# Optimization experiments

Hardware: AMD Instinct MI355X
Metric: run time of the kernel (lower is better)

Reference implementation:

```python
import jax, jax.numpy as jnp
import numpy as np

WS = 7  # window_size
NH = 8  # num_heads

def _rel_pos_index(ws):
    coords = np.stack(np.meshgrid(np.arange(ws), np.arange(ws), indexing='ij'))  # [2,ws,ws]
    flat = coords.reshape(2, -1)                      # [2, ws*ws]
    rel = (flat[:, :, None] - flat[:, None, :]).transpose(1, 2, 0)  # [ws*ws, ws*ws, 2]
    rel = rel + (ws - 1)
    rel[:, :, 0] *= 2 * ws - 1
    return rel.sum(-1)  # [ws*ws, ws*ws]

REL_IDX = jnp.asarray(_rel_pos_index(WS))


def setup_inputs() -> dict:
    key = jax.random.key(0)
    k1, k2, k3 = jax.random.split(key, 3)
    B, H, W, C = 4, 224, 224, 256
    x = jax.random.normal(k1, (B, H * W, C), dtype=jnp.float32)
    nW = (H // WS) * (W // WS)
    mask = jnp.zeros((nW, WS * WS, WS * WS), dtype=jnp.float32)
    qkv_w = jax.random.normal(k2, (3 * C, C), dtype=jnp.float32) * 0.02
    qkv_b = jnp.zeros((3 * C,), dtype=jnp.float32)
    rel_bias_table = jax.random.normal(k3, ((2 * WS - 1) ** 2, NH), dtype=jnp.float32) * 0.02
    return {"x": x, "mask": mask, "qkv_w": qkv_w, "qkv_b": qkv_b,
            "rel_bias_table": rel_bias_table, "H": H, "W": W}


def reference(x, mask, qkv_w, qkv_b, rel_bias_table, H, W):
    B, N, C = x.shape
    nh = rel_bias_table.shape[1]
    hd = C // nh
    scale = hd ** (-0.5)
    shift = WS // 2

    qkv = x @ qkv_w.T + qkv_b                       # [B, N, 3C]
    q = qkv.reshape(B, H, W, 3 * C)
    pad_h = (WS - H % WS) % WS
    pad_w = (WS - W % WS) % WS
    if pad_h or pad_w:
        q = jnp.pad(q, ((0, 0), (0, pad_h), (0, pad_w), (0, 0)))
    Hp, Wp = H + pad_h, W + pad_w

    # mask is provided -> shifted-window path (cyclic shift)
    q = jnp.roll(q, (-shift, -shift), axis=(1, 2))

    nWh, nWw = Hp // WS, Wp // WS
    win = q.reshape(B, nWh, WS, nWw, WS, 3 * C).transpose(0, 1, 3, 2, 4, 5)
    win = win.reshape(B * nWh * nWw, WS * WS, 3, nh, hd).transpose(2, 0, 3, 1, 4)
    qh, kh, vh = win[0], win[1], win[2]             # each [B_, nh, 49, hd]

    attn = jnp.einsum('bhqd,bhkd->bhqk', qh, kh) * scale
    bias = rel_bias_table[REL_IDX.reshape(-1)].reshape(WS * WS, WS * WS, nh)
    attn = attn + bias.transpose(2, 0, 1)[None]     # [B_, nh, 49, 49]

    nW = mask.shape[0]
    attn = attn.reshape(B, nW, nh, WS * WS, WS * WS) + mask[None, :, None]
    attn = jax.nn.softmax(attn.reshape(-1, nh, WS * WS, WS * WS), axis=-1)

    out = jnp.einsum('bhqk,bhkd->bhqd', attn, vh)   # [B_, nh, 49, hd]
    out = out.transpose(0, 2, 1, 3).reshape(-1, WS * WS, C)

    # window reverse
    out = out.reshape(B, nWh, nWw, WS, WS, C).transpose(0, 1, 3, 2, 4, 5)
    out = out.reshape(B, Hp, Wp, C)
    out = jnp.roll(out, (shift, shift), axis=(1, 2))
    return out.reshape(B, Hp * Wp, C)[:, :N, :]
```

## Files before the change

kernel.cpp:

```cpp
#include <hip/hip_runtime.h>
#include <hip/hip_bf16.h>

#define NTOK  49
#define CDIM  256
#define NHD   8
#define HDIM  32
#define HP    224
#define WPW   224
#define SHIFT 3

typedef __attribute__((ext_vector_type(8))) short short8;
typedef __attribute__((ext_vector_type(4))) short short4v;
typedef __attribute__((ext_vector_type(4))) float float4v;

static __device__ __forceinline__ short f2bf(float f) {
    unsigned u = __float_as_uint(f);
    u += 0x7FFF + ((u >> 16) & 1);
    return (short)(u >> 16);
}

__global__ void cvt_w_kernel(const float* __restrict__ w, short* __restrict__ wb) {
    int t = blockIdx.x * 256 + threadIdx.x;
    float4v f = *(const float4v*)(w + (size_t)t * 4);
    short4v o;
    o.x = f2bf(f.x); o.y = f2bf(f.y); o.z = f2bf(f.z); o.w = f2bf(f.w);
    *(short4v*)(wb + (size_t)t * 4) = o;
}

struct __align__(16) SMem {
    int   nsrc[64];
    short xs[8 * 49 * 40];
    float btabt[8 * 169];
    float pad_[8];
    struct {
        union {
            struct { short q[49 * 40]; short k[49 * 40]; } qk;
            short p[64 * 40];
            float o[49 * 36];
        } r1;
        short vT[32 * 72];
    } wv[2];
};

__global__ __launch_bounds__(128, 1)
void swin_attn_kernel(const float* __restrict__ x,
                      const float* __restrict__ mask,
                      const float* __restrict__ qkv_b,
                      const float* __restrict__ btab,
                      const short* __restrict__ wb,
                      float* __restrict__ out)
{
    __shared__ SMem S;

    const int tid = threadIdx.x;
    const int blk = blockIdx.x;
    const int b   = blk >> 10;
    const int wi  = blk & 1023;
    const int wh  = wi >> 5, ww = wi & 31;

    if (tid < NTOK) {
        int i = tid / 7, j = tid - i * 7;
        int hs = wh * 7 + i + SHIFT;  if (hs >= HP)  hs -= HP;
        int wsx = ww * 7 + j + SHIFT; if (wsx >= WPW) wsx -= WPW;
        S.nsrc[tid] = hs * WPW + wsx;
    }
    for (int idx = tid; idx < 1152; idx += 128) {
        ((int*)S.wv[0].vT)[idx] = 0;
        ((int*)S.wv[1].vT)[idx] = 0;
    }
    __syncthreads();

    const size_t xbase = (size_t)b * (HP * WPW) * CDIM;
    for (int idx = tid; idx < NTOK * 64; idx += 128) {
        int r = idx >> 6, k4 = idx & 63;
        float4v f = *(const float4v*)(x + xbase + (size_t)S.nsrc[r] * CDIM + k4 * 4);
        short4v o4;
        o4.x = f2bf(f.x); o4.y = f2bf(f.y); o4.z = f2bf(f.z); o4.w = f2bf(f.w);
        int kt = k4 >> 3, kk = (k4 & 7) * 4;
        *(short4v*)&S.xs[(kt * 49 + r) * 40 + kk] = o4;
    }
    for (int idx = tid; idx < 1352; idx += 128) {
        int h2 = idx & 7, bi = idx >> 3;
        S.btabt[h2 * 169 + bi] = btab[idx];
    }
    __syncthreads();

    const int lane = tid & 63;
    const int w    = tid >> 6;
    const int n16  = lane & 15;
    const int quad = lane >> 4;
    const float scale = 0.17677669529663687f;

    auto& W = S.wv[w];

    int rt[4][4], ct[4];
#pragma unroll
    for (int mt = 0; mt < 4; ++mt)
#pragma unroll
        for (int reg = 0; reg < 4; ++reg) {
            int r = mt * 16 + quad * 4 + reg;
            int i1 = r / 7;
            rt[mt][reg] = i1 * 13 + (r - i1 * 7);
        }
#pragma unroll
    for (int nt = 0; nt < 4; ++nt) {
        int c = nt * 16 + n16;
        int i2 = c / 7;
        ct[nt] = i2 * 13 + (c - i2 * 7) - 84;
    }

    float mreg[4][4][4];
    {
        const float* maskp = mask + (size_t)wi * 2401;
#pragma unroll
        for (int mt = 0; mt < 4; ++mt)
#pragma unroll
            for (int reg = 0; reg < 4; ++reg) {
                int r  = mt * 16 + quad * 4 + reg;
                int rm = (r < NTOK) ? r : (NTOK - 1);
#pragma unroll
                for (int nt = 0; nt < 4; ++nt) {
                    int c  = nt * 16 + n16;
                    int cm = (c < NTOK) ? c : (NTOK - 1);
                    mreg[mt][nt][reg] = maskp[rm * 49 + cm];
                }
            }
    }

#pragma unroll 1
    for (int h = w * 4; h < w * 4 + 4; ++h) {
        const short* bp[6];
        float bias[6];
#pragma unroll
        for (int i = 0; i < 6; ++i) {
            int chan = (i >> 1) * 256 + h * 32 + (i & 1) * 16 + n16;
            bp[i]   = wb + (size_t)chan * 256 + quad * 8;
            bias[i] = qkv_b[chan];
        }
        float4v acc[4][6];
#pragma unroll
        for (int mt = 0; mt < 4; ++mt)
#pragma unroll
            for (int i = 0; i < 6; ++i)
                acc[mt][i] = (float4v)0.0f;

#pragma unroll
        for (int kt = 0; kt < 8; ++kt) {
            short8 a[4];
#pragma unroll
            for (int mt = 0; mt < 4; ++mt)
                a[mt] = *(const short8*)&S.xs[(kt * 49 + mt * 16 + n16) * 40 + quad * 8];
#pragma unroll
            for (int i = 0; i < 6; ++i) {
                short8 bb = *(const short8*)(bp[i] + kt * 32);
#pragma unroll
                for (int mt = 0; mt < 4; ++mt)
                    acc[mt][i] = __builtin_amdgcn_mfma_f32_16x16x32_bf16(a[mt], bb, acc[mt][i], 0, 0, 0);
            }
        }

#pragma unroll
        for (int mt = 0; mt < 4; ++mt)
#pragma unroll
            for (int reg = 0; reg < 4; ++reg) {
                int r = mt * 16 + quad * 4 + reg;
                if (r < NTOK) {
#pragma unroll
                    for (int i = 0; i < 6; ++i) {
                        float v = acc[mt][i][reg] + bias[i];
                        int c = (i & 1) * 16 + n16;
                        if ((i >> 1) == 0)      W.r1.qk.q[r * 40 + c] = f2bf(v * scale);
                        else if ((i >> 1) == 1) W.r1.qk.k[r * 40 + c] = f2bf(v);
                        else                    W.vT[c * 72 + r]      = f2bf(v);
                    }
                }
            }
        __syncthreads();

        short8 aq[4], bk[4];
#pragma unroll
        for (int t = 0; t < 4; ++t) {
            aq[t] = *(const short8*)&W.r1.qk.q[(t * 16 + n16) * 40 + quad * 8];
            bk[t] = *(const short8*)&W.r1.qk.k[(t * 16 + n16) * 40 + quad * 8];
        }
        float4v sa[4][4];
#pragma unroll
        for (int mt = 0; mt < 4; ++mt)
#pragma unroll
            for (int nt = 0; nt < 4; ++nt)
                sa[mt][nt] = __builtin_amdgcn_mfma_f32_16x16x32_bf16(aq[mt], bk[nt], (float4v)0.0f, 0, 0, 0);

        const float* bt = &S.btabt[h * 169];
#pragma unroll
        for (int mt = 0; mt < 4; ++mt)
#pragma unroll
            for (int nt = 0; nt < 4; ++nt)
#pragma unroll
                for (int reg = 0; reg < 4; ++reg) {
                    float sv;
                    if (nt == 3 && n16 >= 1) sv = -1e30f;
                    else {
                        int bidx = rt[mt][reg] - ct[nt];
                        bidx = (bidx > 168) ? 168 : bidx;
                        sv = sa[mt][nt][reg] + bt[bidx] + mreg[mt][nt][reg];
                    }
                    sa[mt][nt][reg] = sv;
                }

#pragma unroll
        for (int mt = 0; mt < 4; ++mt)
#pragma unroll
            for (int reg = 0; reg < 4; ++reg) {
                float m0 = fmaxf(fmaxf(sa[mt][0][reg], sa[mt][1][reg]),
                                 fmaxf(sa[mt][2][reg], sa[mt][3][reg]));
#pragma unroll
                for (int d = 1; d < 16; d <<= 1) m0 = fmaxf(m0, __shfl_xor(m0, d));
                float s0 = 0.f;
#pragma unroll
                for (int nt = 0; nt < 4; ++nt) {
                    float e = __expf(sa[mt][nt][reg] - m0);
                    sa[mt][nt][reg] = e;
                    s0 += e;
                }
#pragma unroll
                for (int d = 1; d < 16; d <<= 1) s0 += __shfl_xor(s0, d);
                float inv = 1.0f / s0;
#pragma unroll
                for (int nt = 0; nt < 4; ++nt) sa[mt][nt][reg] *= inv;
            }

#pragma unroll
        for (int mt = 0; mt < 4; ++mt)
#pragma unroll
            for (int reg = 0; reg < 4; ++reg) {
                int q = mt * 16 + quad * 4 + reg;
                W.r1.p[q * 40 + n16]      = f2bf(sa[mt][0][reg]);
                W.r1.p[q * 40 + 16 + n16] = f2bf(sa[mt][1][reg]);
            }
        __syncthreads();

        float4v oa[2][4];
#pragma unroll
        for (int mtv = 0; mtv < 2; ++mtv)
#pragma unroll
            for (int nt = 0; nt < 4; ++nt)
                oa[mtv][nt] = (float4v)0.0f;

        {
            short8 av[2], bpv[4];
#pragma unroll
            for (int mtv = 0; mtv < 2; ++mtv)
                av[mtv] = *(const short8*)&W.vT[(mtv * 16 + n16) * 72 + quad * 8];
#pragma unroll
            for (int nt = 0; nt < 4; ++nt)
                bpv[nt] = *(const short8*)&W.r1.p[(nt * 16 + n16) * 40 + quad * 8];
#pragma unroll
            for (int mtv = 0; mtv < 2; ++mtv)
#pragma unroll
                for (int nt = 0; nt < 4; ++nt)
                    oa[mtv][nt] = __builtin_amdgcn_mfma_f32_16x16x32_bf16(av[mtv], bpv[nt], oa[mtv][nt], 0, 0, 0);
        }
        __syncthreads();

#pragma unroll
        for (int mt = 0; mt < 4; ++mt)
#pragma unroll
            for (int reg = 0; reg < 4; ++reg) {
                int q = mt * 16 + quad * 4 + reg;
                W.r1.p[q * 40 + n16]      = f2bf(sa[mt][2][reg]);
                W.r1.p[q * 40 + 16 + n16] = f2bf(sa[mt][3][reg]);
            }
        __syncthreads();

        {
            short8 av[2], bpv[4];
#pragma unroll
            for (int mtv = 0; mtv < 2; ++mtv)
                av[mtv] = *(const short8*)&W.vT[(mtv * 16 + n16) * 72 + 32 + quad * 8];
#pragma unroll
            for (int nt = 0; nt < 4; ++nt)
                bpv[nt] = *(const short8*)&W.r1.p[(nt * 16 + n16) * 40 + quad * 8];
#pragma unroll
            for (int mtv = 0; mtv < 2; ++mtv)
#pragma unroll
                for (int nt = 0; nt < 4; ++nt)
                    oa[mtv][nt] = __builtin_amdgcn_mfma_f32_16x16x32_bf16(av[mtv], bpv[nt], oa[mtv][nt], 0, 0, 0);
        }
        __syncthreads();

#pragma unroll
        for (int mtv = 0; mtv < 2; ++mtv)
#pragma unroll
            for (int nt = 0; nt < 4; ++nt)
#pragma unroll
                for (int reg = 0; reg < 4; ++reg) {
                    int qv = nt * 16 + n16;
                    if (qv < NTOK)
                        W.r1.o[qv * 36 + mtv * 16 + quad * 4 + reg] = oa[mtv][nt][reg];
                }
        __syncthreads();
#pragma unroll
        for (int it = 0; it < 7; ++it) {
            int idx = it * 64 + lane;
            if (idx < NTOK * 8) {
                int tok = idx >> 3, c8 = idx & 7;
                float4v ov = *(const float4v*)&W.r1.o[tok * 36 + c8 * 4];
                *(float4v*)(out + xbase + (size_t)S.nsrc[tok] * CDIM + h * HDIM + c8 * 4) = ov;
            }
        }
        __syncthreads();
    }
}

extern "C" void kernel_launch(void* const* d_in, const int* in_sizes, int n_in,
                              void* d_out, int out_size, void* d_ws, size_t ws_size,
                              hipStream_t stream) {
    const float* x      = (const float*)d_in[0];
    const float* mask   = (const float*)d_in[1];
    const float* qkv_w  = (const float*)d_in[2];
    const float* qkv_b  = (const float*)d_in[3];
    const float* btab   = (const float*)d_in[4];
    float* out = (float*)d_out;
    short* wb  = (short*)d_ws;

    cvt_w_kernel<<<dim3(192), dim3(256), 0, stream>>>(qkv_w, wb);
    swin_attn_kernel<<<dim3(4096), dim3(128), 0, stream>>>(
        x, mask, qkv_b, btab, wb, out);
}
```

Before: 950.1 us.

## Make waves independent, swizzle LDS tiles, transpose score layout for in-thread softmax

Each wave now works only on its own LDS region, so block-wide __syncthreads calls between per-head stages become compiler-only memory fences. The attention scores are computed as K·Qᵀ so that most of each softmax reduction happens inside a thread, with only two cross-lane shuffles. The full 64-wide P tile is written once instead of in two halves. The x tile and the P tile use XOR swizzling to cut LDS bank conflicts, and the bias table is stored in LDS as bf16. The risks are correctness that now depends on in-order LDS access within a wave, and small precision loss in the relative position bias.

```diff
diff --git a/kernel.cpp b/kernel.cpp
--- a/kernel.cpp
+++ b/kernel.cpp
@@ -13,10 +13,15 @@
 typedef __attribute__((ext_vector_type(4))) short short4v;
 typedef __attribute__((ext_vector_type(4))) float float4v;
 
+#define MEMFENCE asm volatile("" ::: "memory")
+
 static __device__ __forceinline__ short f2bf(float f) {
     unsigned u = __float_as_uint(f);
     u += 0x7FFF + ((u >> 16) & 1);
     return (short)(u >> 16);
+}
+static __device__ __forceinline__ float bf2f(unsigned short s) {
+    return __uint_as_float((unsigned)s << 16);
 }
 
 __global__ void cvt_w_kernel(const float* __restrict__ w, short* __restrict__ wb) {
@@ -29,13 +34,12 @@
 
 struct __align__(16) SMem {
     int   nsrc[64];
-    short xs[8 * 49 * 40];
-    float btabt[8 * 169];
-    float pad_[8];
-    struct {
+    short xs[8 * 49 * 32];
+    unsigned short btabt[8 * 169];
+    struct WV {
         union {
             struct { short q[49 * 40]; short k[49 * 40]; } qk;
-            short p[64 * 40];
+            short p[64 * 64];
             float o[49 * 36];
         } r1;
         short vT[32 * 72];
@@ -58,16 +62,17 @@
     const int wi  = blk & 1023;
     const int wh  = wi >> 5, ww = wi & 31;
 
+    const int lane = tid & 63;
+    const int w    = tid >> 6;
+    SMem::WV& W = S.wv[w];
+
     if (tid < NTOK) {
         int i = tid / 7, j = tid - i * 7;
         int hs = wh * 7 + i + SHIFT;  if (hs >= HP)  hs -= HP;
         int wsx = ww * 7 + j + SHIFT; if (wsx >= WPW) wsx -= WPW;
         S.nsrc[tid] = hs * WPW + wsx;
     }
-    for (int idx = tid; idx < 1152; idx += 128) {
-        ((int*)S.wv[0].vT)[idx] = 0;
-        ((int*)S.wv[1].vT)[idx] = 0;
-    }
+    for (int i2 = lane; i2 < 1152; i2 += 64) ((int*)W.vT)[i2] = 0;
     __syncthreads();
 
     const size_t xbase = (size_t)b * (HP * WPW) * CDIM;
@@ -76,53 +81,51 @@
         float4v f = *(const float4v*)(x + xbase + (size_t)S.nsrc[r] * CDIM + k4 * 4);
         short4v o4;
         o4.x = f2bf(f.x); o4.y = f2bf(f.y); o4.z = f2bf(f.z); o4.w = f2bf(f.w);
-        int kt = k4 >> 3, kk = (k4 & 7) * 4;
-        *(short4v*)&S.xs[(kt * 49 + r) * 40 + kk] = o4;
+        int kt = k4 >> 3;
+        int iu = ((k4 >> 1) & 3) ^ ((r >> 1) & 3) ^ ((kt >> 1) & 3);
+        *(short4v*)&S.xs[((kt * 49 + r) << 5) + (iu << 3) + ((k4 & 1) << 2)] = o4;
     }
     for (int idx = tid; idx < 1352; idx += 128) {
         int h2 = idx & 7, bi = idx >> 3;
-        S.btabt[h2 * 169 + bi] = btab[idx];
+        S.btabt[h2 * 169 + bi] = (unsigned short)f2bf(btab[idx]);
     }
     __syncthreads();
 
-    const int lane = tid & 63;
-    const int w    = tid >> 6;
     const int n16  = lane & 15;
     const int quad = lane >> 4;
+    const int rs   = (n16 >> 1) & 3;
     const float scale = 0.17677669529663687f;
 
-    auto& W = S.wv[w];
-
-    int rt[4][4], ct[4];
-#pragma unroll
-    for (int mt = 0; mt < 4; ++mt)
+    int qv[4], kv[4][4];
+#pragma unroll
+    for (int ct = 0; ct < 4; ++ct) {
+        int qq = ct * 16 + n16;
+        int qi = qq / 7;
+        qv[ct] = qi * 13 + (qq - qi * 7);
+    }
+#pragma unroll
+    for (int rt = 0; rt < 4; ++rt)
 #pragma unroll
         for (int reg = 0; reg < 4; ++reg) {
-            int r = mt * 16 + quad * 4 + reg;
-            int i1 = r / 7;
-            rt[mt][reg] = i1 * 13 + (r - i1 * 7);
-        }
-#pragma unroll
-    for (int nt = 0; nt < 4; ++nt) {
-        int c = nt * 16 + n16;
-        int i2 = c / 7;
-        ct[nt] = i2 * 13 + (c - i2 * 7) - 84;
-    }
+            int kk = rt * 16 + quad * 4 + reg;
+            int ki = kk / 7;
+            kv[rt][reg] = ki * 13 + (kk - ki * 7);
+        }
 
     float mreg[4][4][4];
     {
         const float* maskp = mask + (size_t)wi * 2401;
 #pragma unroll
-        for (int mt = 0; mt < 4; ++mt)
+        for (int rt = 0; rt < 4; ++rt)
 #pragma unroll
             for (int reg = 0; reg < 4; ++reg) {
-                int r  = mt * 16 + quad * 4 + reg;
-                int rm = (r < NTOK) ? r : (NTOK - 1);
-#pragma unroll
-                for (int nt = 0; nt < 4; ++nt) {
-                    int c  = nt * 16 + n16;
-                    int cm = (c < NTOK) ? c : (NTOK - 1);
-                    mreg[mt][nt][reg] = maskp[rm * 49 + cm];
+                int kk = rt * 16 + quad * 4 + reg;
+                int km = (kk < NTOK) ? kk : (NTOK - 1);
+#pragma unroll
+                for (int ct = 0; ct < 4; ++ct) {
+                    int qq = ct * 16 + n16;
+                    int qm = (qq < NTOK) ? qq : (NTOK - 1);
+                    mreg[rt][ct][reg] = maskp[qm * 49 + km];
                 }
             }
     }
@@ -146,10 +149,13 @@
 
 #pragma unroll
         for (int kt = 0; kt < 8; ++kt) {
+            const int ku = (kt >> 1) & 3;
             short8 a[4];
 #pragma unroll
-            for (int mt = 0; mt < 4; ++mt)
-                a[mt] = *(const short8*)&S.xs[(kt * 49 + mt * 16 + n16) * 40 + quad * 8];
+            for (int mt = 0; mt < 4; ++mt) {
+                int row = mt * 16 + n16;
+                a[mt] = *(const short8*)&S.xs[((kt * 49 + row) << 5) + ((quad ^ rs ^ ku) << 3)];
+            }
 #pragma unroll
             for (int i = 0; i < 6; ++i) {
                 short8 bb = *(const short8*)(bp[i] + kt * 32);
@@ -165,79 +171,88 @@
             for (int reg = 0; reg < 4; ++reg) {
                 int r = mt * 16 + quad * 4 + reg;
                 if (r < NTOK) {
-#pragma unroll
-                    for (int i = 0; i < 6; ++i) {
-                        float v = acc[mt][i][reg] + bias[i];
-                        int c = (i & 1) * 16 + n16;
-                        if ((i >> 1) == 0)      W.r1.qk.q[r * 40 + c] = f2bf(v * scale);
-                        else if ((i >> 1) == 1) W.r1.qk.k[r * 40 + c] = f2bf(v);
-                        else                    W.vT[c * 72 + r]      = f2bf(v);
-                    }
-                }
-            }
-        __syncthreads();
-
-        short8 aq[4], bk[4];
+                    unsigned q0 = (unsigned short)f2bf((acc[mt][0][reg] + bias[0]) * scale);
+                    unsigned q1 = (unsigned short)f2bf((acc[mt][1][reg] + bias[1]) * scale);
+                    *(unsigned*)&W.r1.qk.q[r * 40 + 2 * n16] = q0 | (q1 << 16);
+                    unsigned k0 = (unsigned short)f2bf(acc[mt][2][reg] + bias[2]);
+                    unsigned k1 = (unsigned short)f2bf(acc[mt][3][reg] + bias[3]);
+                    *(unsigned*)&W.r1.qk.k[r * 40 + 2 * n16] = k0 | (k1 << 16);
+                    W.vT[n16 * 72 + r]        = f2bf(acc[mt][4][reg] + bias[4]);
+                    W.vT[(16 + n16) * 72 + r] = f2bf(acc[mt][5][reg] + bias[5]);
+                }
+            }
+        MEMFENCE;
+
+        short8 ak[4], bq[4];
 #pragma unroll
         for (int t = 0; t < 4; ++t) {
-            aq[t] = *(const short8*)&W.r1.qk.q[(t * 16 + n16) * 40 + quad * 8];
-            bk[t] = *(const short8*)&W.r1.qk.k[(t * 16 + n16) * 40 + quad * 8];
+            ak[t] = *(const short8*)&W.r1.qk.k[(t * 16 + n16) * 40 + quad * 8];
+            bq[t] = *(const short8*)&W.r1.qk.q[(t * 16 + n16) * 40 + quad * 8];
         }
         float4v sa[4][4];
 #pragma unroll
-        for (int mt = 0; mt < 4; ++mt)
-#pragma unroll
-            for (int nt = 0; nt < 4; ++nt)
-                sa[mt][nt] = __builtin_amdgcn_mfma_f32_16x16x32_bf16(aq[mt], bk[nt], (float4v)0.0f, 0, 0, 0);
-
-        const float* bt = &S.btabt[h * 169];
-#pragma unroll
-        for (int mt = 0; mt < 4; ++mt)
-#pragma unroll
-            for (int nt = 0; nt < 4; ++nt)
+        for (int rt = 0; rt < 4; ++rt)
+#pragma unroll
+            for (int ct = 0; ct < 4; ++ct)
+                sa[rt][ct] = __builtin_amdgcn_mfma_f32_16x16x32_bf16(ak[rt], bq[ct], (float4v)0.0f, 0, 0, 0);
+
+#pragma unroll
+        for (int rt = 0; rt < 4; ++rt)
+#pragma unroll
+            for (int ct = 0; ct < 4; ++ct)
 #pragma unroll
                 for (int reg = 0; reg < 4; ++reg) {
                     float sv;
-                    if (nt == 3 && n16 >= 1) sv = -1e30f;
+                    if (rt == 3 && !(quad == 0 && reg == 0)) sv = -1e30f;
                     else {
-                        int bidx = rt[mt][reg] - ct[nt];
+                        int bidx = qv[ct] - kv[rt][reg] + 84;
                         bidx = (bidx > 168) ? 168 : bidx;
-                        sv = sa[mt][nt][reg] + bt[bidx] + mreg[mt][nt][reg];
+                        sv = sa[rt][ct][reg] + bf2f(S.btabt[h * 169 + bidx]) + mreg[rt][ct][reg];
                     }
-                    sa[mt][nt][reg] = sv;
-                }
-
-#pragma unroll
-        for (int mt = 0; mt < 4; ++mt)
-#pragma unroll
-            for (int reg = 0; reg < 4; ++reg) {
-                float m0 = fmaxf(fmaxf(sa[mt][0][reg], sa[mt][1][reg]),
-                                 fmaxf(sa[mt][2][reg], sa[mt][3][reg]));
-#pragma unroll
-                for (int d = 1; d < 16; d <<= 1) m0 = fmaxf(m0, __shfl_xor(m0, d));
-                float s0 = 0.f;
-#pragma unroll
-                for (int nt = 0; nt < 4; ++nt) {
-                    float e = __expf(sa[mt][nt][reg] - m0);
-                    sa[mt][nt][reg] = e;
+                    sa[rt][ct][reg] = sv;
+                }
+
+#pragma unroll
+        for (int ct = 0; ct < 4; ++ct) {
+            float m0 = sa[0][ct][0];
+#pragma unroll
+            for (int rt = 0; rt < 4; ++rt)
+#pragma unroll
+                for (int reg = 0; reg < 4; ++reg)
+                    m0 = fmaxf(m0, sa[rt][ct][reg]);
+            m0 = fmaxf(m0, __shfl_xor(m0, 16));
+            m0 = fmaxf(m0, __shfl_xor(m0, 32));
+            float s0 = 0.f;
+#pragma unroll
+            for (int rt = 0; rt < 4; ++rt)
+#pragma unroll
+                for (int reg = 0; reg < 4; ++reg) {
+                    float e = __expf(sa[rt][ct][reg] - m0);
+                    sa[rt][ct][reg] = e;
                     s0 += e;
                 }
-#pragma unroll
-                for (int d = 1; d < 16; d <<= 1) s0 += __shfl_xor(s0, d);
-                float inv = 1.0f / s0;
-#pragma unroll
-                for (int nt = 0; nt < 4; ++nt) sa[mt][nt][reg] *= inv;
-            }
-
-#pragma unroll
-        for (int mt = 0; mt < 4; ++mt)
-#pragma unroll
-            for (int reg = 0; reg < 4; ++reg) {
-                int q = mt * 16 + quad * 4 + reg;
-                W.r1.p[q * 40 + n16]      = f2bf(sa[mt][0][reg]);
-                W.r1.p[q * 40 + 16 + n16] = f2bf(sa[mt][1][reg]);
-            }
-        __syncthreads();
+            s0 += __shfl_xor(s0, 16);
+            s0 += __shfl_xor(s0, 32);
+            float inv = 1.0f / s0;
+#pragma unroll
+            for (int rt = 0; rt < 4; ++rt)
+#pragma unroll
+                for (int reg = 0; reg < 4; ++reg)
+                    sa[rt][ct][reg] *= inv;
+        }
+        MEMFENCE;
+
+#pragma unroll
+        for (int ct = 0; ct < 4; ++ct)
+#pragma unroll
+            for (int rt = 0; rt < 4; ++rt) {
+                short4v pw;
+                pw.x = f2bf(sa[rt][ct][0]); pw.y = f2bf(sa[rt][ct][1]);
+                pw.z = f2bf(sa[rt][ct][2]); pw.w = f2bf(sa[rt][ct][3]);
+                int su = (2 * rt + (quad >> 1)) ^ (n16 & 7);
+                *(short4v*)&W.r1.p[((ct * 16 + n16) << 6) + (su << 3) + ((quad & 1) << 2)] = pw;
+            }
+        MEMFENCE;
 
         float4v oa[2][4];
 #pragma unroll
@@ -245,60 +260,36 @@
 #pragma unroll
             for (int nt = 0; nt < 4; ++nt)
                 oa[mtv][nt] = (float4v)0.0f;
-
-        {
+#pragma unroll
+        for (int kt2 = 0; kt2 < 2; ++kt2) {
             short8 av[2], bpv[4];
 #pragma unroll
             for (int mtv = 0; mtv < 2; ++mtv)
-                av[mtv] = *(const short8*)&W.vT[(mtv * 16 + n16) * 72 + quad * 8];
-#pragma unroll
-            for (int nt = 0; nt < 4; ++nt)
-                bpv[nt] = *(const short8*)&W.r1.p[(nt * 16 + n16) * 40 + quad * 8];
+                av[mtv] = *(const short8*)&W.vT[(mtv * 16 + n16) * 72 + kt2 * 32 + quad * 8];
+#pragma unroll
+            for (int nt = 0; nt < 4; ++nt) {
+                int su = (kt2 * 4 + quad) ^ (n16 & 7);
+                bpv[nt] = *(const short8*)&W.r1.p[((nt * 16 + n16) << 6) + (su << 3)];
+            }
 #pragma unroll
             for (int mtv = 0; mtv < 2; ++mtv)
 #pragma unroll
                 for (int nt = 0; nt < 4; ++nt)
                     oa[mtv][nt] = __builtin_amdgcn_mfma_f32_16x16x32_bf16(av[mtv], bpv[nt], oa[mtv][nt], 0, 0, 0);
         }
-        __syncthreads();
-
-#pragma unroll
-        for (int mt = 0; mt < 4; ++mt)
-#pragma unroll
-            for (int reg = 0; reg < 4; ++reg) {
-                int q = mt * 16 + quad * 4 + reg;
-                W.r1.p[q * 40 + n16]      = f2bf(sa[mt][2][reg]);
-                W.r1.p[q * 40 + 16 + n16] = f2bf(sa[mt][3][reg]);
-            }
-        __syncthreads();
-
-        {
-            short8 av[2], bpv[4];
-#pragma unroll
-            for (int mtv = 0; mtv < 2; ++mtv)
-                av[mtv] = *(const short8*)&W.vT[(mtv * 16 + n16) * 72 + 32 + quad * 8];
+        MEMFENCE;
+
+#pragma unroll
+        for (int mtv = 0; mtv < 2; ++mtv)
 #pragma unroll
             for (int nt = 0; nt < 4; ++nt)
-                bpv[nt] = *(const short8*)&W.r1.p[(nt * 16 + n16) * 40 + quad * 8];
-#pragma unroll
-            for (int mtv = 0; mtv < 2; ++mtv)
-#pragma unroll
-                for (int nt = 0; nt < 4; ++nt)
-                    oa[mtv][nt] = __builtin_amdgcn_mfma_f32_16x16x32_bf16(av[mtv], bpv[nt], oa[mtv][nt], 0, 0, 0);
-        }
-        __syncthreads();
-
-#pragma unroll
-        for (int mtv = 0; mtv < 2; ++mtv)
-#pragma unroll
-            for (int nt = 0; nt < 4; ++nt)
 #pragma unroll
                 for (int reg = 0; reg < 4; ++reg) {
-                    int qv = nt * 16 + n16;
-                    if (qv < NTOK)
-                        W.r1.o[qv * 36 + mtv * 16 + quad * 4 + reg] = oa[mtv][nt][reg];
-                }
-        __syncthreads();
+                    int qvq = nt * 16 + n16;
+                    if (qvq < NTOK)
+                        W.r1.o[qvq * 36 + mtv * 16 + quad * 4 + reg] = oa[mtv][nt][reg];
+                }
+        MEMFENCE;
 #pragma unroll
         for (int it = 0; it < 7; ++it) {
             int idx = it * 64 + lane;
@@ -308,7 +299,7 @@
                 *(float4v*)(out + xbase + (size_t)S.nsrc[tok] * CDIM + h * HDIM + c8 * 4) = ov;
             }
         }
-        __syncthreads();
+        MEMFENCE;
     }
 }
 
```

Measured after the change: 847.5 us. -10.8%, faster.
